# Kernel optimization log

Measured on AMD Instinct MI355X. Metric: run time of the kernel, lower is better.

Reference implementation:

```python
import jax, jax.numpy as jnp
import numpy as np

WS = 8            # window_size
HEADS = 4
HEAD_DIM = 32
DISP = WS // 2    # cyclic shift displacement
TAU = 0.02       # created fresh each forward in the torch code -> constant
NEG = float('-inf')


def _rel_ind():
    idx = np.array([[i, j] for i in range(WS) for j in range(WS)])
    d = idx[None, :, :] - idx[:, None, :]
    return d + WS - 1  # (WS^2, WS^2, 2), values in [0, 2*WS-2]


def _tb_mask():
    m = np.zeros((WS * WS, WS * WS), np.float32)
    m[-DISP * WS:, :-DISP * WS] = NEG
    m[:-DISP * WS, -DISP * WS:] = NEG
    return m


def _lr_mask():
    m = np.zeros((WS, WS, WS, WS), np.float32)
    m[:, -DISP:, :, :-DISP] = NEG
    m[:, :-DISP, :, -DISP:] = NEG
    return m.reshape(WS * WS, WS * WS)


_REL = jnp.asarray(_rel_ind())
_TB = jnp.asarray(_tb_mask())
_LR = jnp.asarray(_lr_mask())


def setup_inputs() -> dict:
    key = jax.random.key(0)
    ks = jax.random.split(key, 5)
    return {
        'x': jax.random.normal(ks[0], (16, 128, 128, 128), jnp.float32),
        'w_qkv': jax.random.normal(ks[1], (384, 128), jnp.float32) * 0.05,
        'w_out': jax.random.normal(ks[2], (128, 128), jnp.float32) * 0.05,
        'b_out': jax.random.normal(ks[3], (128,), jnp.float32) * 0.05,
        'pos_emb': jax.random.normal(ks[4], (15, 15), jnp.float32),
    }


def reference(x, w_qkv, w_out, b_out, pos_emb):
    B, H, W, C = x.shape
    nwh, nww = H // WS, W // WS
    nwin, n = nwh * nww, WS * WS

    x = jnp.roll(x, (-DISP, -DISP), axis=(1, 2))  # cyclic shift
    qkv = x @ w_qkv.T                              # (B,H,W,3*inner)
    q, k, v = jnp.split(qkv, 3, axis=-1)

    def to_win(t):  # (B,H,W,heads*d) -> (B,heads,nwin,n,d)
        t = t.reshape(B, nwh, WS, nww, WS, HEADS, HEAD_DIM)
        return t.transpose(0, 5, 1, 3, 2, 4, 6).reshape(B, HEADS, nwin, n, HEAD_DIM)

    q, k, v = to_win(q), to_win(k), to_win(v)

    def l2n(t):  # F.normalize(p=2, dim=-1), eps=1e-12
        nrm = jnp.sqrt(jnp.sum(t * t, axis=-1, keepdims=True))
        return t / jnp.maximum(nrm, 1e-12)

    q, k = l2n(q), l2n(k)
    dots = jnp.einsum('bhwid,bhwjd->bhwij', q, k) / TAU

    # relative position bias gather
    dots = dots + pos_emb[_REL[:, :, 0], _REL[:, :, 1]]

    # shifted-window masks, applied per window index
    wmask = jnp.zeros((nwin, n, n), jnp.float32)
    wmask = wmask.at[-nww:].add(_TB)
    wmask = wmask.at[nww - 1::nww].add(_LR)
    dots = dots + wmask  # broadcast over (B, heads)

    attn = jax.nn.softmax(dots, axis=-1)
    out = jnp.einsum('bhwij,bhwjd->bhwid', attn, v)

    # windows -> spatial
    out = out.reshape(B, HEADS, nwh, nww, WS, WS, HEAD_DIM)
    out = out.transpose(0, 2, 4, 3, 5, 1, 6).reshape(B, H, W, HEADS * HEAD_DIM)

    out = out @ w_out.T + b_out
    out = jnp.roll(out, (DISP, DISP), axis=(1, 2))  # reverse cyclic shift
    return out
```

## Files before the change

kernel.cpp:

```cpp
#include <hip/hip_runtime.h>
#include <math.h>


typedef short     bs8 __attribute__((ext_vector_type(8)));
typedef _Float16  hs8 __attribute__((ext_vector_type(8)));
typedef float     f4_t __attribute__((ext_vector_type(4)));
typedef short     s4_t __attribute__((ext_vector_type(4)));
typedef _Float16  h4_t __attribute__((ext_vector_type(4)));

union B8 { s4_t s[2]; bs8 b; hs8 h; };

#define MFB(a,b,c) __builtin_amdgcn_mfma_f32_16x16x32_bf16(a,b,c,0,0,0)
#define MFH(a,b,c) __builtin_amdgcn_mfma_f32_16x16x32_f16(a,b,c,0,0,0)

#define XH_O   0
#define XL_O   17408
#define WH_O   34816
#define WL_O   87040
#define QH_O   0
#define QL_O   18432
#define KH_O   36864
#define KL_O   55296
#define VT_O   73728
#define P_O    91136
#define OH_O   125952
#define OL_O   142848
#define WOH_O  0
#define WOL_O  34816
#define PE_O   159744
#define SCL_O  160656
#define LDS_BYTES 162704

#define IMG 128
#define DISP 4

__device__ __forceinline__ unsigned short f2bf(float f) {
    unsigned u = __float_as_uint(f);
    return (unsigned short)((u + 0x7FFFu + ((u >> 16) & 1u)) >> 16);
}
__device__ __forceinline__ float bf2f(unsigned short s) {
    return __uint_as_float(((unsigned)s) << 16);
}

__global__ __launch_bounds__(512, 2)
void swin_window_attn(const float* __restrict__ x,
                      const float* __restrict__ w_qkv,
                      const float* __restrict__ w_out,
                      const float* __restrict__ b_out,
                      const float* __restrict__ pos_emb,
                      float* __restrict__ out)
{
    __shared__ __align__(16) char LB[LDS_BYTES];
    #define PTR(off) (LB + (off))

    const int t   = threadIdx.x;
    const int bid = blockIdx.x;
    const int bi  = bid >> 8;
    const int wy  = (bid >> 4) & 15;
    const int wx  = bid & 15;
    const int l   = t & 63;
    const int wv  = t >> 6;
    const int li  = l & 15;
    const int lg  = l >> 4;

    {
        const float* xb = x + (size_t)bi * (IMG * IMG * 128);
        #pragma unroll
        for (int it = 0; it < 4; ++it) {
            int idx = t + it * 512;
            int tok = idx >> 5;
            int f4  = (idx & 31) << 2;
            int gr = ((wy << 3) + (tok >> 3) + DISP) & 127;
            int gc = ((wx << 3) + (tok & 7) + DISP) & 127;
            float4 v4 = *(const float4*)(xb + (gr * IMG + gc) * 128 + f4);
            unsigned short h0 = f2bf(v4.x), h1 = f2bf(v4.y), h2 = f2bf(v4.z), h3 = f2bf(v4.w);
            s4_t hv = { (short)h0, (short)h1, (short)h2, (short)h3 };
            s4_t lv = { (short)f2bf(v4.x - bf2f(h0)), (short)f2bf(v4.y - bf2f(h1)),
                        (short)f2bf(v4.z - bf2f(h2)), (short)f2bf(v4.w - bf2f(h3)) };
            *(s4_t*)(PTR(XH_O) + (tok * 136 + f4) * 2) = hv;
            *(s4_t*)(PTR(XL_O) + (tok * 136 + f4) * 2) = lv;
        }
        if (t < 225) ((float*)PTR(PE_O))[t] = pos_emb[t];
    }
    __syncthreads();

    const int mtp = wv >> 2;
    const int ntq = wv & 3;
    f4_t acc[12];
    #pragma unroll
    for (int i = 0; i < 12; ++i) acc[i] = (f4_t){0.f, 0.f, 0.f, 0.f};

    #pragma unroll
    for (int hf = 0; hf < 2; ++hf) {
        #pragma unroll
        for (int it = 0; it < 12; ++it) {
            int idx = t + it * 512;
            int o   = idx >> 5;
            int f4  = (idx & 31) << 2;
            float4 v4 = *(const float4*)(w_qkv + (size_t)(hf * 192 + o) * 128 + f4);
            unsigned short h0 = f2bf(v4.x), h1 = f2bf(v4.y), h2 = f2bf(v4.z), h3 = f2bf(v4.w);
            s4_t hv = { (short)h0, (short)h1, (short)h2, (short)h3 };
            s4_t lv = { (short)f2bf(v4.x - bf2f(h0)), (short)f2bf(v4.y - bf2f(h1)),
                        (short)f2bf(v4.z - bf2f(h2)), (short)f2bf(v4.w - bf2f(h3)) };
            *(s4_t*)(PTR(WH_O) + (o * 136 + f4) * 2) = hv;
            *(s4_t*)(PTR(WL_O) + (o * 136 + f4) * 2) = lv;
        }
        __syncthreads();

        #pragma unroll
        for (int ks = 0; ks < 4; ++ks) {
            int koff = ks * 32 + lg * 8;
            bs8 ah[2], al[2];
            #pragma unroll
            for (int m = 0; m < 2; ++m) {
                int row = ((mtp * 2 + m) * 16 + li);
                ah[m] = *(const bs8*)(PTR(XH_O) + (row * 136 + koff) * 2);
                al[m] = *(const bs8*)(PTR(XL_O) + (row * 136 + koff) * 2);
            }
            #pragma unroll
            for (int j = 0; j < 3; ++j) {
                int wrow = (ntq * 3 + j) * 16 + li;
                bs8 bh = *(const bs8*)(PTR(WH_O) + (wrow * 136 + koff) * 2);
                bs8 bl = *(const bs8*)(PTR(WL_O) + (wrow * 136 + koff) * 2);
                #pragma unroll
                for (int m = 0; m < 2; ++m) {
                    int ai = hf * 6 + j * 2 + m;
                    acc[ai] = MFB(ah[m], bh, acc[ai]);
                    acc[ai] = MFB(ah[m], bl, acc[ai]);
                    acc[ai] = MFB(al[m], bh, acc[ai]);
                }
            }
        }
        __syncthreads();
    }

    #pragma unroll
    for (int hf = 0; hf < 2; ++hf)
        #pragma unroll
        for (int j = 0; j < 3; ++j)
            #pragma unroll
            for (int m = 0; m < 2; ++m) {
                int ch   = hf * 192 + (ntq * 3 + j) * 16 + li;
                int tokb = (mtp * 2 + m) * 16 + lg * 4;
                f4_t vv  = acc[hf * 6 + j * 2 + m];
                if (ch < 256) {
                    int isK = ch >> 7;
                    int hh  = (ch >> 5) & 3;
                    int d   = ch & 31;
                    char* ph = PTR(isK ? KH_O : QH_O) + ((hh * 64 + tokb) * 36 + d) * 2;
                    char* pl = PTR(isK ? KL_O : QL_O) + ((hh * 64 + tokb) * 36 + d) * 2;
                    #pragma unroll
                    for (int r = 0; r < 4; ++r) {
                        float q = vv[r];
                        unsigned short hi = f2bf(q);
                        *(short*)(ph + r * 72) = (short)hi;
                        *(short*)(pl + r * 72) = (short)f2bf(q - bf2f(hi));
                    }
                } else {
                    int hh = (ch >> 5) & 3;
                    int d  = ch & 31;
                    h4_t p4 = { (_Float16)vv[0], (_Float16)vv[1],
                                (_Float16)vv[2], (_Float16)vv[3] };
                    *(h4_t*)(PTR(VT_O) + ((hh * 32 + d) * 68 + tokb) * 2) = p4;
                }
            }

    float4 wo_pref[8];
    #pragma unroll
    for (int it = 0; it < 8; ++it) {
        int idx = t + it * 512;
        wo_pref[it] = *(const float4*)(w_out + (size_t)(idx >> 5) * 128 + ((idx & 31) << 2));
    }
    const int mtp2 = wv & 1, ntq2 = wv >> 1;
    float bpref[2];
    bpref[0] = b_out[(2 * ntq2 + 0) * 16 + li];
    bpref[1] = b_out[(2 * ntq2 + 1) * 16 + li];
    __syncthreads();

    {
        int qk = t >> 8, hh = (t >> 6) & 3, tok = t & 63;
        const char* bh = PTR(qk ? KH_O : QH_O) + (hh * 64 + tok) * 72;
        const char* bl = PTR(qk ? KL_O : QL_O) + (hh * 64 + tok) * 72;
        float s = 0.f;
        #pragma unroll
        for (int e8 = 0; e8 < 8; ++e8) {
            s4_t a = *(const s4_t*)(bh + e8 * 8);
            s4_t b = *(const s4_t*)(bl + e8 * 8);
            #pragma unroll
            for (int c = 0; c < 4; ++c) {
                float v = bf2f((unsigned short)a[c]) + bf2f((unsigned short)b[c]);
                s += v * v;
            }
        }
        float sc = (qk ? 1.f : 50.f) / fmaxf(sqrtf(s), 1e-12f);
        ((float*)PTR(SCL_O))[qk * 256 + hh * 64 + tok] = sc;
    }
    __syncthreads();

    const int hh = wv >> 1;
    const int cc = wv & 1;
    {
        B8 qa[2][2];
        #pragma unroll
        for (int m = 0; m < 2; ++m) {
            int row = (2 * cc + m) * 16 + li;
            const char* bq = PTR(QH_O) + ((hh * 64 + row) * 36 + lg * 8) * 2;
            const char* cq = PTR(QL_O) + ((hh * 64 + row) * 36 + lg * 8) * 2;
            qa[m][0].s[0] = *(const s4_t*)(bq); qa[m][0].s[1] = *(const s4_t*)(bq + 8);
            qa[m][1].s[0] = *(const s4_t*)(cq); qa[m][1].s[1] = *(const s4_t*)(cq + 8);
        }
        f4_t sa[2][4];
        #pragma unroll
        for (int m = 0; m < 2; ++m)
            #pragma unroll
            for (int nt = 0; nt < 4; ++nt) sa[m][nt] = (f4_t){0.f, 0.f, 0.f, 0.f};
        #pragma unroll
        for (int nt = 0; nt < 4; ++nt) {
            int krow = nt * 16 + li;
            const char* bk = PTR(KH_O) + ((hh * 64 + krow) * 36 + lg * 8) * 2;
            const char* ck = PTR(KL_O) + ((hh * 64 + krow) * 36 + lg * 8) * 2;
            B8 kh, kl;
            kh.s[0] = *(const s4_t*)(bk); kh.s[1] = *(const s4_t*)(bk + 8);
            kl.s[0] = *(const s4_t*)(ck); kl.s[1] = *(const s4_t*)(ck + 8);
            #pragma unroll
            for (int m = 0; m < 2; ++m) {
                sa[m][nt] = MFB(qa[m][0].b, kh.b, sa[m][nt]);
                sa[m][nt] = MFB(qa[m][0].b, kl.b, sa[m][nt]);
                sa[m][nt] = MFB(qa[m][1].b, kh.b, sa[m][nt]);
            }
        }

        const float* scl = (const float*)PTR(SCL_O);
        const float* pef = (const float*)PTR(PE_O);
        float skv[4];
        #pragma unroll
        for (int nt = 0; nt < 4; ++nt) skv[nt] = scl[256 + hh * 64 + nt * 16 + li];
        #pragma unroll
        for (int m = 0; m < 2; ++m)
            #pragma unroll
            for (int r = 0; r < 4; ++r) {
                int i = (2 * cc + m) * 16 + lg * 4 + r;
                float sqv = scl[hh * 64 + i];
                int ri = i >> 3, ci = i & 7;
                float vals[4];
                #pragma unroll
                for (int nt = 0; nt < 4; ++nt) {
                    int col = nt * 16 + li;
                    int rj = col >> 3, cj = col & 7;
                    float bias = pef[(rj - ri + 7) * 15 + (cj - ci + 7)];
                    bool msk = ((wy == 15) && ((i >= 32) != (col >= 32)))
                            || ((wx == 15) && ((ci >= 4) != ((cj & 7) >= 4)));
                    vals[nt] = msk ? -1e30f : (sa[m][nt][r] * sqv * skv[nt] + bias);
                }
                float mx = fmaxf(fmaxf(vals[0], vals[1]), fmaxf(vals[2], vals[3]));
                #pragma unroll
                for (int off = 1; off < 16; off <<= 1) mx = fmaxf(mx, __shfl_xor(mx, off, 16));
                float e0 = __expf(vals[0] - mx), e1 = __expf(vals[1] - mx);
                float e2 = __expf(vals[2] - mx), e3 = __expf(vals[3] - mx);
                float sum = (e0 + e1) + (e2 + e3);
                #pragma unroll
                for (int off = 1; off < 16; off <<= 1) sum += __shfl_xor(sum, off, 16);
                float inv = 1.0f / sum;
                char* prow = PTR(P_O) + ((hh * 64 + i) * 68 + li) * 2;
                *(_Float16*)(prow)      = (_Float16)(e0 * inv);
                *(_Float16*)(prow + 32) = (_Float16)(e1 * inv);
                *(_Float16*)(prow + 64) = (_Float16)(e2 * inv);
                *(_Float16*)(prow + 96) = (_Float16)(e3 * inv);
            }

        f4_t oa[2][2];
        #pragma unroll
        for (int m = 0; m < 2; ++m)
            #pragma unroll
            for (int nv = 0; nv < 2; ++nv) oa[m][nv] = (f4_t){0.f, 0.f, 0.f, 0.f};
        #pragma unroll
        for (int kv = 0; kv < 2; ++kv) {
            B8 pa[2], vb[2];
            #pragma unroll
            for (int m = 0; m < 2; ++m) {
                int row = (2 * cc + m) * 16 + li;
                const char* pp = PTR(P_O) + ((hh * 64 + row) * 68 + kv * 32 + lg * 8) * 2;
                pa[m].s[0] = *(const s4_t*)(pp); pa[m].s[1] = *(const s4_t*)(pp + 8);
            }
            #pragma unroll
            for (int nv = 0; nv < 2; ++nv) {
                int d = nv * 16 + li;
                const char* vp = PTR(VT_O) + ((hh * 32 + d) * 68 + kv * 32 + lg * 8) * 2;
                vb[nv].s[0] = *(const s4_t*)(vp); vb[nv].s[1] = *(const s4_t*)(vp + 8);
            }
            #pragma unroll
            for (int m = 0; m < 2; ++m)
                #pragma unroll
                for (int nv = 0; nv < 2; ++nv)
                    oa[m][nv] = MFH(pa[m].h, vb[nv].h, oa[m][nv]);
        }
        #pragma unroll
        for (int m = 0; m < 2; ++m)
            #pragma unroll
            for (int nv = 0; nv < 2; ++nv)
                #pragma unroll
                for (int r = 0; r < 4; ++r) {
                    int tokr = (2 * cc + m) * 16 + lg * 4 + r;
                    int d = hh * 32 + nv * 16 + li;
                    float val = oa[m][nv][r];
                    unsigned short hi = f2bf(val);
                    *(short*)(PTR(OH_O) + (tokr * 132 + d) * 2) = (short)hi;
                    *(short*)(PTR(OL_O) + (tokr * 132 + d) * 2) = (short)f2bf(val - bf2f(hi));
                }
    }
    __syncthreads();

    #pragma unroll
    for (int it = 0; it < 8; ++it) {
        int idx = t + it * 512;
        int o   = idx >> 5;
        int f4  = (idx & 31) << 2;
        float4 v4 = wo_pref[it];
        unsigned short h0 = f2bf(v4.x), h1 = f2bf(v4.y), h2 = f2bf(v4.z), h3 = f2bf(v4.w);
        s4_t hv = { (short)h0, (short)h1, (short)h2, (short)h3 };
        s4_t lv = { (short)f2bf(v4.x - bf2f(h0)), (short)f2bf(v4.y - bf2f(h1)),
                    (short)f2bf(v4.z - bf2f(h2)), (short)f2bf(v4.w - bf2f(h3)) };
        *(s4_t*)(PTR(WOH_O) + (o * 136 + f4) * 2) = hv;
        *(s4_t*)(PTR(WOL_O) + (o * 136 + f4) * 2) = lv;
    }
    __syncthreads();

    {
        f4_t pc[2][2];
        #pragma unroll
        for (int m = 0; m < 2; ++m)
            #pragma unroll
            for (int jj = 0; jj < 2; ++jj) pc[m][jj] = (f4_t){0.f, 0.f, 0.f, 0.f};
        #pragma unroll
        for (int ks = 0; ks < 4; ++ks) {
            int koff = ks * 32 + lg * 8;
            B8 oh[2], ol[2];
            #pragma unroll
            for (int m = 0; m < 2; ++m) {
                int row = (2 * mtp2 + m) * 16 + li;
                const char* po = PTR(OH_O) + (row * 132 + koff) * 2;
                const char* qo = PTR(OL_O) + (row * 132 + koff) * 2;
                oh[m].s[0] = *(const s4_t*)(po); oh[m].s[1] = *(const s4_t*)(po + 8);
                ol[m].s[0] = *(const s4_t*)(qo); ol[m].s[1] = *(const s4_t*)(qo + 8);
            }
            #pragma unroll
            for (int jj = 0; jj < 2; ++jj) {
                int wrow = (2 * ntq2 + jj) * 16 + li;
                bs8 bh = *(const bs8*)(PTR(WOH_O) + (wrow * 136 + koff) * 2);
                bs8 bl = *(const bs8*)(PTR(WOL_O) + (wrow * 136 + koff) * 2);
                #pragma unroll
                for (int m = 0; m < 2; ++m) {
                    pc[m][jj] = MFB(oh[m].b, bh, pc[m][jj]);
                    pc[m][jj] = MFB(oh[m].b, bl, pc[m][jj]);
                    pc[m][jj] = MFB(ol[m].b, bh, pc[m][jj]);
                }
            }
        }
        float* ob = out + (size_t)bi * (IMG * IMG * 128);
        #pragma unroll
        for (int m = 0; m < 2; ++m)
            #pragma unroll
            for (int jj = 0; jj < 2; ++jj) {
                int chn = (2 * ntq2 + jj) * 16 + li;
                float bb = bpref[jj];
                #pragma unroll
                for (int r = 0; r < 4; ++r) {
                    int tokr = (2 * mtp2 + m) * 16 + lg * 4 + r;
                    int gr = ((wy << 3) + (tokr >> 3) + DISP) & 127;
                    int gc = ((wx << 3) + (tokr & 7) + DISP) & 127;
                    ob[(gr * IMG + gc) * 128 + chn] = pc[m][jj][r] + bb;
                }
            }
    }
}

extern "C" void kernel_launch(void* const* d_in, const int* in_sizes, int n_in,
                              void* d_out, int out_size, void* d_ws, size_t ws_size,
                              hipStream_t stream) {
    const float* x       = (const float*)d_in[0];
    const float* w_qkv   = (const float*)d_in[1];
    const float* w_out   = (const float*)d_in[2];
    const float* b_out   = (const float*)d_in[3];
    const float* pos_emb = (const float*)d_in[4];
    float* outp = (float*)d_out;

    swin_window_attn<<<dim3(4096), dim3(512), 0, stream>>>(
        x, w_qkv, w_out, b_out, pos_emb, outp);
}
```

Measured before the change: 482.1 us.

## Pre-split weights once and stream them into LDS with direct global-to-LDS loads

Adds a small prep kernel that converts w_qkv and w_out into padded bf16 hi/lo layouts in workspace, once per call. The main kernel then copies these pre-split tiles straight into LDS with global_load_lds, instead of converting the fp32 weights in every one of the 4096 blocks. The first half of w_qkv is loaded alongside the x tile, and the w_out load is moved earlier so it overlaps the softmax and PV phase. This removes per-block conversion ALU work and register staging, at the cost of an extra kernel launch and more reliance on correct LDS aliasing and barrier placement.

```diff
diff --git a/kernel.cpp b/kernel.cpp
--- a/kernel.cpp
+++ b/kernel.cpp
@@ -31,6 +31,9 @@
 #define SCL_O  160656
 #define LDS_BYTES 162704
 
+#define WSQ_O  0
+#define WSO_O  208896
+
 #define IMG 128
 #define DISP 4
 
@@ -41,11 +44,50 @@
 __device__ __forceinline__ float bf2f(unsigned short s) {
     return __uint_as_float(((unsigned)s) << 16);
 }
+__device__ __forceinline__ void gload16(const void* g, void* l) {
+    __builtin_amdgcn_global_load_lds(
+        (const __attribute__((address_space(1))) unsigned int*)g,
+        (__attribute__((address_space(3))) unsigned int*)l, 16, 0, 0);
+}
+
+__global__ __launch_bounds__(256)
+void prep_weights(const float* __restrict__ w_qkv,
+                  const float* __restrict__ w_out,
+                  char* __restrict__ ws)
+{
+    int idx = blockIdx.x * 256 + threadIdx.x;
+    int row = idx / 34;
+    int g   = idx - row * 34;
+    int e   = g << 2;
+    const float* src;
+    char *dh, *dl;
+    if (row < 384) {
+        int hf = row >= 192;
+        int r  = row - hf * 192;
+        src = w_qkv + (size_t)row * 128;
+        dh = ws + WSQ_O + hf * 104448 + r * 272;
+        dl = dh + 52224;
+    } else {
+        int r = row - 384;
+        src = w_out + (size_t)r * 128;
+        dh = ws + WSO_O + r * 272;
+        dl = dh + 34816;
+    }
+    s4_t hv = {0, 0, 0, 0}, lv = {0, 0, 0, 0};
+    if (e < 128) {
+        float4 v4 = *(const float4*)(src + e);
+        unsigned short h0 = f2bf(v4.x), h1 = f2bf(v4.y), h2 = f2bf(v4.z), h3 = f2bf(v4.w);
+        hv = (s4_t){ (short)h0, (short)h1, (short)h2, (short)h3 };
+        lv = (s4_t){ (short)f2bf(v4.x - bf2f(h0)), (short)f2bf(v4.y - bf2f(h1)),
+                     (short)f2bf(v4.z - bf2f(h2)), (short)f2bf(v4.w - bf2f(h3)) };
+    }
+    *(s4_t*)(dh + e * 2) = hv;
+    *(s4_t*)(dl + e * 2) = lv;
+}
 
 __global__ __launch_bounds__(512, 2)
 void swin_window_attn(const float* __restrict__ x,
-                      const float* __restrict__ w_qkv,
-                      const float* __restrict__ w_out,
+                      const char*  __restrict__ ws,
                       const float* __restrict__ b_out,
                       const float* __restrict__ pos_emb,
                       float* __restrict__ out)
@@ -62,6 +104,15 @@
     const int wv  = t >> 6;
     const int li  = l & 15;
     const int lg  = l >> 4;
+
+    {
+        const char* wsrc = ws + WSQ_O;
+        #pragma unroll
+        for (int i = 0; i < 13; ++i) {
+            int c = wv + i * 8;
+            if (c < 102) gload16(wsrc + c * 1024 + (l << 4), PTR(WH_O) + c * 1024);
+        }
+    }
 
     {
         const float* xb = x + (size_t)bi * (IMG * IMG * 128);
@@ -90,23 +141,7 @@
     #pragma unroll
     for (int i = 0; i < 12; ++i) acc[i] = (f4_t){0.f, 0.f, 0.f, 0.f};
 
-    #pragma unroll
-    for (int hf = 0; hf < 2; ++hf) {
-        #pragma unroll
-        for (int it = 0; it < 12; ++it) {
-            int idx = t + it * 512;
-            int o   = idx >> 5;
-            int f4  = (idx & 31) << 2;
-            float4 v4 = *(const float4*)(w_qkv + (size_t)(hf * 192 + o) * 128 + f4);
-            unsigned short h0 = f2bf(v4.x), h1 = f2bf(v4.y), h2 = f2bf(v4.z), h3 = f2bf(v4.w);
-            s4_t hv = { (short)h0, (short)h1, (short)h2, (short)h3 };
-            s4_t lv = { (short)f2bf(v4.x - bf2f(h0)), (short)f2bf(v4.y - bf2f(h1)),
-                        (short)f2bf(v4.z - bf2f(h2)), (short)f2bf(v4.w - bf2f(h3)) };
-            *(s4_t*)(PTR(WH_O) + (o * 136 + f4) * 2) = hv;
-            *(s4_t*)(PTR(WL_O) + (o * 136 + f4) * 2) = lv;
-        }
-        __syncthreads();
-
+    auto gemm_half = [&](int hf) {
         #pragma unroll
         for (int ks = 0; ks < 4; ++ks) {
             int koff = ks * 32 + lg * 8;
@@ -131,8 +166,21 @@
                 }
             }
         }
-        __syncthreads();
-    }
+    };
+
+    gemm_half(0);
+    __syncthreads();
+    {
+        const char* wsrc = ws + WSQ_O + 104448;
+        #pragma unroll
+        for (int i = 0; i < 13; ++i) {
+            int c = wv + i * 8;
+            if (c < 102) gload16(wsrc + c * 1024 + (l << 4), PTR(WH_O) + c * 1024);
+        }
+    }
+    __syncthreads();
+    gemm_half(1);
+    __syncthreads();
 
     #pragma unroll
     for (int hf = 0; hf < 2; ++hf)
@@ -165,12 +213,6 @@
                 }
             }
 
-    float4 wo_pref[8];
-    #pragma unroll
-    for (int it = 0; it < 8; ++it) {
-        int idx = t + it * 512;
-        wo_pref[it] = *(const float4*)(w_out + (size_t)(idx >> 5) * 128 + ((idx & 31) << 2));
-    }
     const int mtp2 = wv & 1, ntq2 = wv >> 1;
     float bpref[2];
     bpref[0] = b_out[(2 * ntq2 + 0) * 16 + li];
@@ -199,6 +241,7 @@
 
     const int hh = wv >> 1;
     const int cc = wv & 1;
+    f4_t sa[2][4];
     {
         B8 qa[2][2];
         #pragma unroll
@@ -209,7 +252,6 @@
             qa[m][0].s[0] = *(const s4_t*)(bq); qa[m][0].s[1] = *(const s4_t*)(bq + 8);
             qa[m][1].s[0] = *(const s4_t*)(cq); qa[m][1].s[1] = *(const s4_t*)(cq + 8);
         }
-        f4_t sa[2][4];
         #pragma unroll
         for (int m = 0; m < 2; ++m)
             #pragma unroll
@@ -229,7 +271,19 @@
                 sa[m][nt] = MFB(qa[m][1].b, kh.b, sa[m][nt]);
             }
         }
-
+    }
+    __syncthreads();
+
+    {
+        const char* wsrc = ws + WSO_O;
+        #pragma unroll
+        for (int i = 0; i < 9; ++i) {
+            int c = wv + i * 8;
+            if (c < 68) gload16(wsrc + c * 1024 + (l << 4), PTR(WOH_O) + c * 1024);
+        }
+    }
+
+    {
         const float* scl = (const float*)PTR(SCL_O);
         const float* pef = (const float*)PTR(PE_O);
         float skv[4];
@@ -307,21 +361,6 @@
                     *(short*)(PTR(OH_O) + (tokr * 132 + d) * 2) = (short)hi;
                     *(short*)(PTR(OL_O) + (tokr * 132 + d) * 2) = (short)f2bf(val - bf2f(hi));
                 }
-    }
-    __syncthreads();
-
-    #pragma unroll
-    for (int it = 0; it < 8; ++it) {
-        int idx = t + it * 512;
-        int o   = idx >> 5;
-        int f4  = (idx & 31) << 2;
-        float4 v4 = wo_pref[it];
-        unsigned short h0 = f2bf(v4.x), h1 = f2bf(v4.y), h2 = f2bf(v4.z), h3 = f2bf(v4.w);
-        s4_t hv = { (short)h0, (short)h1, (short)h2, (short)h3 };
-        s4_t lv = { (short)f2bf(v4.x - bf2f(h0)), (short)f2bf(v4.y - bf2f(h1)),
-                    (short)f2bf(v4.z - bf2f(h2)), (short)f2bf(v4.w - bf2f(h3)) };
-        *(s4_t*)(PTR(WOH_O) + (o * 136 + f4) * 2) = hv;
-        *(s4_t*)(PTR(WOL_O) + (o * 136 + f4) * 2) = lv;
     }
     __syncthreads();
 
@@ -383,7 +422,9 @@
     const float* b_out   = (const float*)d_in[3];
     const float* pos_emb = (const float*)d_in[4];
     float* outp = (float*)d_out;
-
+    char* ws = (char*)d_ws;
+
+    prep_weights<<<dim3(68), dim3(256), 0, stream>>>(w_qkv, w_out, ws);
     swin_window_attn<<<dim3(4096), dim3(512), 0, stream>>>(
-        x, w_qkv, w_out, b_out, pos_emb, outp);
-}
+        x, ws, b_out, pos_emb, outp);
+}
```

Result: faster. 448.6 us (-7.0%).
